# Performance work log

Hardware: AMD Instinct MI355X
Metric: run time of the kernel (lower is better)

Reference implementation:

```python
import jax, jax.numpy as jnp
import numpy as np

N_ROWS = 4096   # output features (N)
M_COLS = 4096   # input features (M)
BATCH = 4096
NNZ_PER_ROW = 819


def setup_inputs() -> dict:
    rng = np.random.default_rng(0)
    # sample NNZ_PER_ROW distinct, sorted column indices per row (CSR structure)
    cols = np.argsort(rng.random((N_ROWS, M_COLS)), axis=1)[:, :NNZ_PER_ROW]
    cols = np.sort(cols, axis=1).reshape(-1).astype(np.int32)            # [nnz]
    row_ids = np.repeat(np.arange(N_ROWS, dtype=np.int32), NNZ_PER_ROW)  # [nnz], expanded indptr

    key = jax.random.key(0)
    k1, k2, k3 = jax.random.split(key, 3)
    inp = jax.random.normal(k1, (BATCH, M_COLS), dtype=jnp.float32)
    W_val = jax.random.normal(k2, (N_ROWS * NNZ_PER_ROW,), dtype=jnp.float32) * 0.02
    bias = jax.random.normal(k3, (N_ROWS,), dtype=jnp.float32)
    return {
        "input": inp,
        "W_val": W_val,
        "bias": bias,
        "row_ids": jnp.asarray(row_ids),
        "cols": jnp.asarray(cols),
        "N": N_ROWS,
    }


def reference(input, W_val, bias, row_ids, cols, N):
    # Faithful math of SparseLinearFunction: y = x @ W^T + bias where W is the
    # CSR matrix (W_val, row_ids, cols) of shape (N, M). Densify via scatter
    # (CSR has unique (row, col) pairs) then use a single GEMM.
    M = input.shape[-1]
    W = jnp.zeros((N, M), dtype=W_val.dtype).at[row_ids, cols].set(W_val)  # [N, M]
    return jnp.matmul(input, W.T) + bias  # [B, N]
```

## Files before the change

### kernel.cpp

```cpp
#include <hip/hip_runtime.h>
#include <hip/hip_bf16.h>
#include <stdint.h>


#define B_DIM 4096
#define M_DIM 4096
#define N_DIM 4096
#define NNZ_ROW 819
#define BK 32

typedef __attribute__((ext_vector_type(8))) __bf16 bf16x8;
typedef __attribute__((ext_vector_type(4))) float f32x4;

__device__ __forceinline__ unsigned short f32_to_bf16(float f) {
    union { float f; unsigned int u; } v;
    v.f = f;
    unsigned int r = v.u + 0x7FFFu + ((v.u >> 16) & 1u);
    return (unsigned short)(r >> 16);
}

__device__ __forceinline__ void load_lds16(const void* g, void* l) {
    __builtin_amdgcn_global_load_lds(
        (const __attribute__((address_space(1))) void*)g,
        (__attribute__((address_space(3))) void*)l,
        16, 0, 0);
}

__global__ __launch_bounds__(256) void densify_w(
    const float* __restrict__ wval,
    const int* __restrict__ cols,
    unsigned short* __restrict__ wb) {
    __shared__ __attribute__((aligned(16))) unsigned short row_s[M_DIM];
    const int row = blockIdx.x;
    const int tid = threadIdx.x;
    uint4* rs4 = (uint4*)row_s;
    rs4[tid]       = make_uint4(0u, 0u, 0u, 0u);
    rs4[tid + 256] = make_uint4(0u, 0u, 0u, 0u);
    __syncthreads();
    const size_t base = (size_t)row * NNZ_ROW;
    for (int j = tid; j < NNZ_ROW; j += 256) {
        const int c = cols[base + j];
        row_s[c] = f32_to_bf16(wval[base + j]);
    }
    __syncthreads();
    uint4* dst = (uint4*)(wb + (size_t)row * M_DIM);
    dst[tid]       = rs4[tid];
    dst[tid + 256] = rs4[tid + 256];
}

__global__ __launch_bounds__(256) void cvt_x_bf16(
    const float4* __restrict__ x, uint4* __restrict__ y, int n8) {
    int i = blockIdx.x * 256 + threadIdx.x;
    if (i >= n8) return;
    const float4 a = x[2 * i];
    const float4 b = x[2 * i + 1];
    union { ushort ush[8]; uint4 u4; } o;
    o.ush[0] = f32_to_bf16(a.x); o.ush[1] = f32_to_bf16(a.y);
    o.ush[2] = f32_to_bf16(a.z); o.ush[3] = f32_to_bf16(a.w);
    o.ush[4] = f32_to_bf16(b.x); o.ush[5] = f32_to_bf16(b.y);
    o.ush[6] = f32_to_bf16(b.z); o.ush[7] = f32_to_bf16(b.w);
    y[i] = o.u4;
}


__global__ __launch_bounds__(256, 4) void gemm_bt_bias(
    const unsigned short* __restrict__ Xb,
    const unsigned short* __restrict__ Wb,
    const float* __restrict__ bias,
    float* __restrict__ out)
{
    __shared__ __attribute__((aligned(16))) unsigned short As[2 * 128 * BK];
    __shared__ __attribute__((aligned(16))) unsigned short Bs[2 * 128 * BK];

    const int tid    = threadIdx.x;
    const int wid    = tid >> 6;
    const int lane   = tid & 63;
    const int wm     = wid & 1;
    const int wn     = wid >> 1;
    const int lane15 = lane & 15;
    const int laneq  = lane >> 4;

    const int bm0 = blockIdx.y * 128;
    const int bn0 = blockIdx.x * 128;

    const int srow = (lane >> 2);
    const int skof = ((lane & 3) ^ ((lane >> 3) & 3)) * 8;

    const unsigned short* aSrc0 =
        Xb + (size_t)(bm0 + wid * 16 + srow) * M_DIM + skof;
    const unsigned short* aSrc1 = aSrc0 + (size_t)64 * M_DIM;
    const unsigned short* bSrc0 =
        Wb + (size_t)(bn0 + wid * 16 + srow) * M_DIM + skof;
    const unsigned short* bSrc1 = bSrc0 + (size_t)64 * M_DIM;

    const int dOff0 = wid * 512;
    const int dOff1 = (wid + 4) * 512;

    const int slot = (laneq ^ ((lane15 >> 1) & 3)) * 8;
    int aOff[4], bOff[4];
#pragma unroll
    for (int t = 0; t < 4; ++t) {
        aOff[t] = (wm * 64 + t * 16 + lane15) * BK + slot;
        bOff[t] = (wn * 64 + t * 16 + lane15) * BK + slot;
    }

    f32x4 acc[4][4];
#pragma unroll
    for (int i = 0; i < 4; ++i)
#pragma unroll
        for (int j = 0; j < 4; ++j) acc[i][j] = (f32x4)0.0f;

    load_lds16(aSrc0, As + dOff0);
    load_lds16(aSrc1, As + dOff1);
    load_lds16(bSrc0, Bs + dOff0);
    load_lds16(bSrc1, Bs + dOff1);
    __syncthreads();

    int buf = 0;
    for (int kt = 0; kt < M_DIM; kt += BK) {
        const int nbase = (buf ^ 1) * (128 * BK);
        if (kt + BK < M_DIM) {
            load_lds16(aSrc0 + kt + BK, As + nbase + dOff0);
            load_lds16(aSrc1 + kt + BK, As + nbase + dOff1);
            load_lds16(bSrc0 + kt + BK, Bs + nbase + dOff0);
            load_lds16(bSrc1 + kt + BK, Bs + nbase + dOff1);
        }
        const int cbase = buf * (128 * BK);

        bf16x8 af[4], bf[4];
#pragma unroll
        for (int t = 0; t < 4; ++t) {
            af[t] = *((const bf16x8*)(As + cbase + aOff[t]));
            bf[t] = *((const bf16x8*)(Bs + cbase + bOff[t]));
        }
#pragma unroll
        for (int mt = 0; mt < 4; ++mt)
#pragma unroll
            for (int nt = 0; nt < 4; ++nt)
                acc[mt][nt] = __builtin_amdgcn_mfma_f32_16x16x32_bf16(
                    af[mt], bf[nt], acc[mt][nt], 0, 0, 0);

        __syncthreads();
        buf ^= 1;
    }

#pragma unroll
    for (int nt = 0; nt < 4; ++nt) {
        const int col = bn0 + wn * 64 + nt * 16 + lane15;
        const float bv = bias[col];
#pragma unroll
        for (int mt = 0; mt < 4; ++mt) {
            const int row0 = bm0 + wm * 64 + mt * 16 + laneq * 4;
#pragma unroll
            for (int r = 0; r < 4; ++r) {
                out[(size_t)(row0 + r) * N_DIM + col] = acc[mt][nt][r] + bv;
            }
        }
    }
}


extern "C" void kernel_launch(void* const* d_in, const int* in_sizes, int n_in,
                              void* d_out, int out_size, void* d_ws, size_t ws_size,
                              hipStream_t stream) {
    const float* x       = (const float*)d_in[0];
    const float* wval    = (const float*)d_in[1];
    const float* bias    = (const float*)d_in[2];
    const int*   cols    = (const int*)d_in[4];
    float* out = (float*)d_out;

    unsigned short* Wb = (unsigned short*)d_ws;
    unsigned short* Xb = Wb + (size_t)N_DIM * M_DIM;

    densify_w<<<dim3(N_DIM), dim3(256), 0, stream>>>(wval, cols, Wb);
    {
        int n8 = (B_DIM * M_DIM) / 8;
        cvt_x_bf16<<<dim3(n8 / 256), dim3(256), 0, stream>>>(
            (const float4*)x, (uint4*)Xb, n8);
    }
    gemm_bt_bias<<<dim3(N_DIM / 128, B_DIM / 128), dim3(256), 0, stream>>>(
        Xb, Wb, bias, out);
}
```

Baseline: 302.5 us.

## Load W fragments directly from global into registers, bypassing LDS

The B (weight) operand is no longer staged through shared memory. Each lane now loads its bf16x8 MFMA fragments straight from global memory into registers, double-buffered across two K steps, and the main loop is unrolled by two with fixed LDS buffers for A. This halves LDS usage and LDS traffic, but B data shared by the two wm waves is fetched twice from global/L2 and the loads are uncoalesced row-strided accesses. The occupancy hint also drops from 4 to 3 because of the extra registers.

```diff
diff --git a/kernel.cpp b/kernel.cpp
--- a/kernel.cpp
+++ b/kernel.cpp
@@ -63,14 +63,13 @@
 }
 
 
-__global__ __launch_bounds__(256, 4) void gemm_bt_bias(
+__global__ __launch_bounds__(256, 3) void gemm_bt_bias(
     const unsigned short* __restrict__ Xb,
     const unsigned short* __restrict__ Wb,
     const float* __restrict__ bias,
     float* __restrict__ out)
 {
     __shared__ __attribute__((aligned(16))) unsigned short As[2 * 128 * BK];
-    __shared__ __attribute__((aligned(16))) unsigned short Bs[2 * 128 * BK];
 
     const int tid    = threadIdx.x;
     const int wid    = tid >> 6;
@@ -85,23 +84,23 @@
 
     const int srow = (lane >> 2);
     const int skof = ((lane & 3) ^ ((lane >> 3) & 3)) * 8;
-
     const unsigned short* aSrc0 =
         Xb + (size_t)(bm0 + wid * 16 + srow) * M_DIM + skof;
     const unsigned short* aSrc1 = aSrc0 + (size_t)64 * M_DIM;
-    const unsigned short* bSrc0 =
-        Wb + (size_t)(bn0 + wid * 16 + srow) * M_DIM + skof;
-    const unsigned short* bSrc1 = bSrc0 + (size_t)64 * M_DIM;
-
     const int dOff0 = wid * 512;
     const int dOff1 = (wid + 4) * 512;
 
     const int slot = (laneq ^ ((lane15 >> 1) & 3)) * 8;
-    int aOff[4], bOff[4];
+    int aOff[4];
+#pragma unroll
+    for (int t = 0; t < 4; ++t)
+        aOff[t] = (wm * 64 + t * 16 + lane15) * BK + slot;
+
+    const bf16x8* bP[4];
 #pragma unroll
     for (int t = 0; t < 4; ++t) {
-        aOff[t] = (wm * 64 + t * 16 + lane15) * BK + slot;
-        bOff[t] = (wn * 64 + t * 16 + lane15) * BK + slot;
+        const int nrow = bn0 + wn * 64 + t * 16 + lane15;
+        bP[t] = (const bf16x8*)(Wb + (size_t)nrow * M_DIM + laneq * 8);
     }
 
     f32x4 acc[4][4];
@@ -112,36 +111,49 @@
 
     load_lds16(aSrc0, As + dOff0);
     load_lds16(aSrc1, As + dOff1);
-    load_lds16(bSrc0, Bs + dOff0);
-    load_lds16(bSrc1, Bs + dOff1);
+    bf16x8 b0[4], b1[4];
+#pragma unroll
+    for (int t = 0; t < 4; ++t) b0[t] = bP[t][0];
     __syncthreads();
 
-    int buf = 0;
-    for (int kt = 0; kt < M_DIM; kt += BK) {
-        const int nbase = (buf ^ 1) * (128 * BK);
-        if (kt + BK < M_DIM) {
-            load_lds16(aSrc0 + kt + BK, As + nbase + dOff0);
-            load_lds16(aSrc1 + kt + BK, As + nbase + dOff1);
-            load_lds16(bSrc0 + kt + BK, Bs + nbase + dOff0);
-            load_lds16(bSrc1 + kt + BK, Bs + nbase + dOff1);
+    for (int kt = 0; kt < M_DIM; kt += 2 * BK) {
+        load_lds16(aSrc0 + kt + BK, As + 128 * BK + dOff0);
+        load_lds16(aSrc1 + kt + BK, As + 128 * BK + dOff1);
+#pragma unroll
+        for (int t = 0; t < 4; ++t) b1[t] = bP[t][(kt + BK) >> 3];
+        {
+            bf16x8 af[4];
+#pragma unroll
+            for (int t = 0; t < 4; ++t)
+                af[t] = *((const bf16x8*)(As + aOff[t]));
+#pragma unroll
+            for (int mt = 0; mt < 4; ++mt)
+#pragma unroll
+                for (int nt = 0; nt < 4; ++nt)
+                    acc[mt][nt] = __builtin_amdgcn_mfma_f32_16x16x32_bf16(
+                        af[mt], b0[nt], acc[mt][nt], 0, 0, 0);
         }
-        const int cbase = buf * (128 * BK);
+        __syncthreads();
 
-        bf16x8 af[4], bf[4];
+        if (kt + 2 * BK < M_DIM) {
+            load_lds16(aSrc0 + kt + 2 * BK, As + dOff0);
+            load_lds16(aSrc1 + kt + 2 * BK, As + dOff1);
 #pragma unroll
-        for (int t = 0; t < 4; ++t) {
-            af[t] = *((const bf16x8*)(As + cbase + aOff[t]));
-            bf[t] = *((const bf16x8*)(Bs + cbase + bOff[t]));
+            for (int t = 0; t < 4; ++t) b0[t] = bP[t][(kt + 2 * BK) >> 3];
         }
+        {
+            bf16x8 af[4];
 #pragma unroll
-        for (int mt = 0; mt < 4; ++mt)
+            for (int t = 0; t < 4; ++t)
+                af[t] = *((const bf16x8*)(As + 128 * BK + aOff[t]));
 #pragma unroll
-            for (int nt = 0; nt < 4; ++nt)
-                acc[mt][nt] = __builtin_amdgcn_mfma_f32_16x16x32_bf16(
-                    af[mt], bf[nt], acc[mt][nt], 0, 0, 0);
-
+            for (int mt = 0; mt < 4; ++mt)
+#pragma unroll
+                for (int nt = 0; nt < 4; ++nt)
+                    acc[mt][nt] = __builtin_amdgcn_mfma_f32_16x16x32_bf16(
+                        af[mt], b1[nt], acc[mt][nt], 0, 0, 0);
+        }
         __syncthreads();
-        buf ^= 1;
     }
 
 #pragma unroll
```

After: 461.6 us. 52.6% more time.
